# Performance work log

Measured on AMD Instinct MI355X. Metric: run time of the kernel, lower is better.

## Reference

```python
import jax, jax.numpy as jnp
import numpy as np

LMAX, MMAX = 6, 2
M_SIZE = (7, 6, 5)
SPHERE_C, HID = 128, 128
N_NODES, N_EDGES = 5000, 20000
N_COEFF_FULL = (LMAX + 1) ** 2                       # 49, l-primary node coeffs
N_COEFF_M = M_SIZE[0] + 2 * (M_SIZE[1] + M_SIZE[2])  # 29, m-primary edge coeffs
EXTRA_M0 = LMAX * HID                                # gate scalars from conv1


def _gate_idx():
    # maps each gated m-primary coefficient (all but l=0,m=0) to its degree index l-1
    idx = [l - 1 for l in range(1, LMAX + 1)]            # m=0 block (l=1..lmax)
    for m in range(1, MMAX + 1):
        for _ in range(2):                               # (-m, +m) components
            idx += [l - 1 for l in range(m, LMAX + 1)]
    return np.asarray(idx, dtype=np.int32)

GATE_IDX = jnp.asarray(_gate_idx())


def _layer_norm(h, s, b):
    mu = jnp.mean(h, axis=-1, keepdims=True)
    var = jnp.var(h, axis=-1, keepdims=True)
    return (h - mu) * jax.lax.rsqrt(var + 1e-5) * s + b


def _radial(e, w0, b0, s0, bb0, w1, b1, s1, bb1, w2, b2):
    h = jax.nn.silu(_layer_norm(e @ w0 + b0, s0, bb0))
    h = jax.nn.silu(_layer_norm(h @ w1 + b1, s1, bb1))
    return h @ w2 + b2


def _so2_conv(x, w_m0, b_m0, w_m1, w_m2, extra, x_rad=None):
    # x: [E, N_COEFF_M, C_in] in m-primary layout
    E = x.shape[0]
    w_m = (w_m1, w_m2)
    outs = []
    # m = 0: plain linear over flattened (l, channel)
    x0 = x[:, :M_SIZE[0]].reshape(E, -1)
    off_rad = 0
    if x_rad is not None:
        x0 = x0 * x_rad[:, :x0.shape[1]]
        off_rad = x0.shape[1]
    x0 = x0 @ w_m0 + b_m0
    x0_extra = None
    if extra:
        x0_extra, x0 = x0[:, :extra], x0[:, extra:]
    outs.append(x0.reshape(E, M_SIZE[0], -1))
    off = M_SIZE[0]
    # m > 0: complex-style SO(2) convolution per order m
    for m in range(1, MMAX + 1):
        sz = M_SIZE[m]
        xm = x[:, off:off + 2 * sz].reshape(E, 2, -1)    # [E, 2, sz*C_in]
        if x_rad is not None:
            d = xm.shape[2]
            xm = xm * x_rad[:, off_rad:off_rad + d][:, None, :]
            off_rad += d
        y = xm @ w_m[m - 1]                              # [E, 2, 2*sz*C_out]
        half = y.shape[2] // 2
        yr, yi = y[..., :half], y[..., half:]
        out_r = yr[:, 0] - yi[:, 1]
        out_i = yr[:, 1] + yi[:, 0]
        outs.append(jnp.stack((out_r, out_i), axis=1).reshape(E, 2 * sz, -1))
        off += 2 * sz
    out = jnp.concatenate(outs, axis=1)
    return (out, x0_extra) if extra else out


def _gate_act(gating, x):
    # gating: [E, LMAX*HID], x: [E, N_COEFF_M, HID]
    g = jax.nn.sigmoid(gating).reshape(-1, LMAX, HID)[:, GATE_IDX]  # [E, N_COEFF_M-1, HID]
    scalars = jax.nn.silu(x[:, :1])
    return jnp.concatenate((scalars, x[:, 1:] * g), axis=1)


def _edgewise(x, x_edge, edge_index, wig, wig_inv, env, params):
    (rw0, rb0, rs0, rbb0, rw1, rb1, rs1, rbb1, rw2, rb2,
     c1w0, c1b0, c1w1, c1w2, c2w0, c2b0, c2w1, c2w2) = params
    # gather source/target node features and concat channels -> [E, 49, 2C]
    msg = jnp.concatenate((x[edge_index[0]], x[edge_index[1]]), axis=2)
    # Wigner rotation + M mapping: l-primary (49) -> m-primary (29)
    msg = jnp.einsum('emj,ejc->emc', wig, msg)
    x_rad = _radial(x_edge, rw0, rb0, rs0, rbb0, rw1, rb1, rs1, rbb1, rw2, rb2)
    msg, gating = _so2_conv(msg, c1w0, c1b0, c1w1, c1w2, EXTRA_M0, x_rad)
    msg = _gate_act(gating, msg)
    msg = _so2_conv(msg, c2w0, c2b0, c2w1, c2w2, 0)
    msg = msg * env
    # inverse rotation: m-primary (29) -> l-primary (49)
    msg = jnp.einsum('ejm,emc->ejc', wig_inv, msg)
    return jax.ops.segment_sum(msg, edge_index[1], num_segments=x.shape[0])


def setup_inputs() -> dict:
    key = jax.random.key(0)
    ks = iter(jax.random.split(key, 40))
    def W(shape):
        return jax.random.normal(next(ks), shape, jnp.float32) / np.sqrt(shape[0])
    C_IN1 = 2 * SPHERE_C
    rad_out = C_IN1 * sum(M_SIZE)  # 4608
    inp = {}
    inp['x'] = jax.random.normal(next(ks), (N_NODES, N_COEFF_FULL, SPHERE_C), jnp.float32)
    inp['x_edge'] = jax.random.normal(next(ks), (N_EDGES, 128), jnp.float32)
    inp['edge_distance'] = jax.random.uniform(next(ks), (N_EDGES,), jnp.float32, 0.1, 6.0)
    inp['edge_index'] = jax.random.randint(next(ks), (2, N_EDGES), 0, N_NODES)
    inp['wigner_and_M_mapping'] = jax.random.normal(next(ks), (N_EDGES, N_COEFF_M, N_COEFF_FULL), jnp.float32) / np.sqrt(N_COEFF_FULL)
    inp['wigner_and_M_mapping_inv'] = jax.random.normal(next(ks), (N_EDGES, N_COEFF_FULL, N_COEFF_M), jnp.float32) / np.sqrt(N_COEFF_M)
    inp['edge_envelope'] = jax.random.uniform(next(ks), (N_EDGES, 1, 1), jnp.float32)
    inp['rad_w0'] = W((128, 256)); inp['rad_b0'] = jnp.zeros((256,), jnp.float32)
    inp['rad_ln0_s'] = jnp.ones((256,), jnp.float32); inp['rad_ln0_b'] = jnp.zeros((256,), jnp.float32)
    inp['rad_w1'] = W((256, 256)); inp['rad_b1'] = jnp.zeros((256,), jnp.float32)
    inp['rad_ln1_s'] = jnp.ones((256,), jnp.float32); inp['rad_ln1_b'] = jnp.zeros((256,), jnp.float32)
    inp['rad_w2'] = W((256, rad_out)); inp['rad_b2'] = jnp.zeros((rad_out,), jnp.float32)
    inp['c1_w_m0'] = W((M_SIZE[0] * C_IN1, M_SIZE[0] * HID + EXTRA_M0))
    inp['c1_b_m0'] = jnp.zeros((M_SIZE[0] * HID + EXTRA_M0,), jnp.float32)
    inp['c1_w_m1'] = W((M_SIZE[1] * C_IN1, 2 * M_SIZE[1] * HID))
    inp['c1_w_m2'] = W((M_SIZE[2] * C_IN1, 2 * M_SIZE[2] * HID))
    inp['c2_w_m0'] = W((M_SIZE[0] * HID, M_SIZE[0] * SPHERE_C))
    inp['c2_b_m0'] = jnp.zeros((M_SIZE[0] * SPHERE_C,), jnp.float32)
    inp['c2_w_m1'] = W((M_SIZE[1] * HID, 2 * M_SIZE[1] * SPHERE_C))
    inp['c2_w_m2'] = W((M_SIZE[2] * HID, 2 * M_SIZE[2] * SPHERE_C))
    return inp


def reference(x, x_edge, edge_distance, edge_index, wigner_and_M_mapping,
              wigner_and_M_mapping_inv, edge_envelope,
              rad_w0, rad_b0, rad_ln0_s, rad_ln0_b, rad_w1, rad_b1, rad_ln1_s, rad_ln1_b,
              rad_w2, rad_b2, c1_w_m0, c1_b_m0, c1_w_m1, c1_w_m2,
              c2_w_m0, c2_b_m0, c2_w_m1, c2_w_m2):
    # edge_distance is accepted (module signature) but unused in the original forward
    params = (rad_w0, rad_b0, rad_ln0_s, rad_ln0_b, rad_w1, rad_b1, rad_ln1_s, rad_ln1_b,
              rad_w2, rad_b2, c1_w_m0, c1_b_m0, c1_w_m1, c1_w_m2,
              c2_w_m0, c2_b_m0, c2_w_m1, c2_w_m2)
    return _edgewise(x, x_edge, edge_index, wigner_and_M_mapping,
                     wigner_and_M_mapping_inv, edge_envelope, params)
```

## Files before the change

kernel.cpp:

```cpp
#include <hip/hip_runtime.h>
#include <stdint.h>


#define E_NUM   20000
#define NN      5000

typedef uint16_t u16;
typedef __bf16  bf16x8 __attribute__((ext_vector_type(8)));
typedef float   f32x4  __attribute__((ext_vector_type(4)));
typedef uint16_t u16x8 __attribute__((ext_vector_type(8)));

__device__ __forceinline__ float bf2f(u16 h){
  uint32_t u = ((uint32_t)h) << 16;
  return __builtin_bit_cast(float, u);
}
__device__ __forceinline__ u16 f2bf(float f){
  uint32_t u = __builtin_bit_cast(uint32_t, f);
  u += 0x7fffu + ((u >> 16) & 1u);
  return (u16)(u >> 16);
}
__device__ __forceinline__ float sigm(float x){ return 1.f / (1.f + __expf(-x)); }

__device__ __forceinline__ void gload16(const void* g, void* l){
  __builtin_amdgcn_global_load_lds(
      (const __attribute__((address_space(1))) void*)g,
      (__attribute__((address_space(3))) void*)l, 16, 0, 0);
}

__device__ __forceinline__ int swz8(int orig, int nwg){
  int q = nwg >> 3, r = nwg & 7;
  int x = orig & 7, p = orig >> 3;
  int base = (x < r) ? x * (q + 1) : r * (q + 1) + (x - r) * q;
  return base + p;
}

__global__ void k_hist(const int* __restrict__ eidx, int* __restrict__ cnt){
  int e = blockIdx.x * 256 + threadIdx.x;
  if (e < E_NUM) atomicAdd(&cnt[eidx[E_NUM + e]], 1);
}
__global__ __launch_bounds__(256) void k_scan(const int* __restrict__ cnt,
                                              int* __restrict__ off){
  __shared__ int part[256];
  int t = threadIdx.x;
  int s = 0;
  #pragma unroll
  for (int i = 0; i < 20; ++i){
    int idx = t * 20 + i;
    if (idx < NN) s += cnt[idx];
  }
  part[t] = s;
  __syncthreads();
  if (t == 0){
    int run = 0;
    for (int i = 0; i < 256; ++i){ int v = part[i]; part[i] = run; run += v; }
  }
  __syncthreads();
  int run = part[t];
  #pragma unroll
  for (int i = 0; i < 20; ++i){
    int idx = t * 20 + i;
    if (idx < NN){ off[idx] = run; run += cnt[idx]; }
  }
}
__global__ void k_scatter(const int* __restrict__ eidx, int* __restrict__ off,
                          int* __restrict__ perm){
  int e = blockIdx.x * 256 + threadIdx.x;
  if (e < E_NUM){
    int pos = atomicAdd(&off[eidx[E_NUM + e]], 1);
    perm[pos] = e;
  }
}

__global__ void k_transpose_w(const float* __restrict__ in, u16* __restrict__ out,
                              int K, int N){
  __shared__ float t[32][33];
  int nb = blockIdx.x * 32, kb = blockIdx.y * 32;
  int tx = threadIdx.x & 31, ty = threadIdx.x >> 5;
  for (int i = ty; i < 32; i += 8)
    t[i][tx] = in[(size_t)(kb + i) * N + (nb + tx)];
  __syncthreads();
  for (int i = ty; i < 32; i += 8)
    out[(size_t)(nb + i) * K + (kb + tx)] = f2bf(t[tx][i]);
}

__global__ __launch_bounds__(256) void k_xpose(const float* __restrict__ x,
                                               u16* __restrict__ xT){
  __shared__ float t[6272];
  int n = blockIdx.x, tid = threadIdx.x;
  const float* xp = x + (size_t)n * 6272;
  for (int i = tid; i < 6272; i += 256) t[i] = xp[i];
  __syncthreads();
  int c = tid >> 1;
  int kh = (tid & 1) * 32;
  u16* o = xT + (size_t)n * 8192 + c * 64 + kh;
  #pragma unroll
  for (int q = 0; q < 4; ++q){
    u16x8 h;
    #pragma unroll
    for (int i = 0; i < 8; ++i){
      int k = kh + q * 8 + i;
      h[i] = (k < 49) ? f2bf(t[k * 128 + c]) : (u16)0;
    }
    *(u16x8*)(o + q * 8) = h;
  }
}

__global__ void k_gather_xe(const float* __restrict__ x_edge,
                            const int* __restrict__ perm,
                            u16* __restrict__ xe, int e0){
  int el = blockIdx.x, c = threadIdx.x;
  int pe = perm[e0 + el];
  xe[(size_t)el * 128 + c] = f2bf(x_edge[(size_t)pe * 128 + c]);
}

struct Seg {
  const u16* A; const u16* B; u16* C; const float* bias;
  int M, N, K, lda, blk0;
};
struct Seg5 { Seg s[5]; int nwg; };

__device__ __forceinline__ void gemm_tile(
    const u16* __restrict__ A, int lda, const u16* __restrict__ B,
    const float* __restrict__ bias, float* __restrict__ Cf,
    u16* __restrict__ Cb, int ldc, int M, int N, int K,
    int bm, int bn, u16* As , u16* Bs )
{
  const int tid  = threadIdx.x;
  const int lane = tid & 63;
  const int wave = tid >> 6;
  const int wm = wave >> 1, wn = wave & 1;
  const int fr = lane & 15, fq = lane >> 4;
  const int row0 = bm * 128;

  const int lr  = lane >> 2;
  const int lg  = lane & 3;
  const int rA0 = wave * 32 + lr;
  const int rA1 = rA0 + 16;
  const int g0  = lg ^ ((rA0 >> 1) & 3);
  const int g1  = lg ^ ((rA1 >> 1) & 3);
  int gra0 = row0 + rA0; if (gra0 > M - 1) gra0 = M - 1;
  int gra1 = row0 + rA1; if (gra1 > M - 1) gra1 = M - 1;
  const u16* aS0 = A + (size_t)gra0 * lda + g0 * 8;
  const u16* aS1 = A + (size_t)gra1 * lda + g1 * 8;
  const u16* bS0 = B + (size_t)(bn * 128 + rA0) * K + g0 * 8;
  const u16* bS1 = B + (size_t)(bn * 128 + rA1) * K + g1 * 8;
  const int dA0 = (wave * 32) * 32;
  const int dA1 = (wave * 32 + 16) * 32;

  int aoff[4], boff[4];
  #pragma unroll
  for (int mi = 0; mi < 4; ++mi){
    int r = wm * 64 + mi * 16 + fr;
    aoff[mi] = r * 32 + (fq ^ ((r >> 1) & 3)) * 8;
  }
  #pragma unroll
  for (int ni = 0; ni < 4; ++ni){
    int r = wn * 64 + ni * 16 + fr;
    boff[ni] = r * 32 + (fq ^ ((r >> 1) & 3)) * 8;
  }

  f32x4 acc[4][4];
  #pragma unroll
  for (int i = 0; i < 4; ++i)
    #pragma unroll
    for (int j = 0; j < 4; ++j) acc[i][j] = (f32x4){0.f, 0.f, 0.f, 0.f};

  auto stage = [&](int buf, int k0){
    gload16(aS0 + k0, &As[buf * 4096 + dA0]);
    gload16(aS1 + k0, &As[buf * 4096 + dA1]);
    gload16(bS0 + k0, &Bs[buf * 4096 + dA0]);
    gload16(bS1 + k0, &Bs[buf * 4096 + dA1]);
  };

  stage(0, 0);
  __syncthreads();
  int cur = 0;
  for (int k0 = 0; k0 < K; k0 += 32){
    if (k0 + 32 < K) stage(cur ^ 1, k0 + 32);
    bf16x8 af[4], bfv[4];
    #pragma unroll
    for (int mi = 0; mi < 4; ++mi)
      af[mi] = __builtin_bit_cast(bf16x8, *(const u16x8*)&As[cur * 4096 + aoff[mi]]);
    #pragma unroll
    for (int ni = 0; ni < 4; ++ni)
      bfv[ni] = __builtin_bit_cast(bf16x8, *(const u16x8*)&Bs[cur * 4096 + boff[ni]]);
    #pragma unroll
    for (int mi = 0; mi < 4; ++mi)
      #pragma unroll
      for (int ni = 0; ni < 4; ++ni)
        acc[mi][ni] = __builtin_amdgcn_mfma_f32_16x16x32_bf16(af[mi], bfv[ni], acc[mi][ni], 0, 0, 0);
    __syncthreads();
    cur ^= 1;
  }

  #pragma unroll
  for (int ni = 0; ni < 4; ++ni){
    int col = bn * 128 + wn * 64 + ni * 16 + fr;
    float bv = bias ? bias[col] : 0.f;
    #pragma unroll
    for (int mi = 0; mi < 4; ++mi){
      #pragma unroll
      for (int i = 0; i < 4; ++i){
        int row = row0 + wm * 64 + mi * 16 + fq * 4 + i;
        if (row < M){
          float v = acc[mi][ni][i] + bv;
          if (Cb) Cb[(size_t)row * ldc + col] = f2bf(v);
          else    Cf[(size_t)row * ldc + col] = v;
        }
      }
    }
  }
}

__global__ __launch_bounds__(256) void k_gemm_bt(
    const u16* __restrict__ A, int lda, const u16* __restrict__ B,
    const float* __restrict__ bias, float* __restrict__ Cf,
    u16* __restrict__ Cb, int ldc, int M, int N, int K)
{
  __shared__ u16 As[2 * 4096];
  __shared__ u16 Bs[2 * 4096];
  gemm_tile(A, lda, B, bias, Cf, Cb, ldc, M, N, K,
            blockIdx.y, blockIdx.x, As, Bs);
}

__global__ __launch_bounds__(256) void k_gemm_seg(Seg5 g)
{
  __shared__ u16 As[2 * 4096];
  __shared__ u16 Bs[2 * 4096];
  int wgid = swz8(blockIdx.x, g.nwg);
  Seg sg = g.s[4];
  if (wgid < g.s[4].blk0) sg = g.s[3];
  if (wgid < g.s[3].blk0) sg = g.s[2];
  if (wgid < g.s[2].blk0) sg = g.s[1];
  if (wgid < g.s[1].blk0) sg = g.s[0];
  int local = wgid - sg.blk0;
  int nbx = sg.N >> 7;
  int bn = local % nbx;
  int bm = local / nbx;
  gemm_tile(sg.A, sg.lda, sg.B, sg.bias, nullptr, sg.C, sg.N,
            sg.M, sg.N, sg.K, bm, bn, As, Bs);
}

__global__ __launch_bounds__(256) void k_ln_silu(
    const float* __restrict__ in, const float* __restrict__ sc,
    const float* __restrict__ bb, u16* __restrict__ out)
{
  int e = blockIdx.x, t = threadIdx.x;
  float v = in[(size_t)e * 256 + t];
  float s1 = v, s2 = v * v;
  #pragma unroll
  for (int off = 32; off > 0; off >>= 1){
    s1 += __shfl_down(s1, off);
    s2 += __shfl_down(s2, off);
  }
  __shared__ float r1[4], r2[4];
  if ((t & 63) == 0){ r1[t >> 6] = s1; r2[t >> 6] = s2; }
  __syncthreads();
  float S1 = r1[0] + r1[1] + r1[2] + r1[3];
  float S2 = r2[0] + r2[1] + r2[2] + r2[3];
  float mu  = S1 * (1.f / 256.f);
  float var = S2 * (1.f / 256.f) - mu * mu;
  float nv = (v - mu) * rsqrtf(var + 1e-5f) * sc[t] + bb[t];
  out[(size_t)e * 256 + t] = f2bf(nv * sigm(nv));
}

__global__ __launch_bounds__(256) void k_wig_fwd(
    const u16* __restrict__ xT, const int* __restrict__ eidx,
    const float* __restrict__ wig, const u16* __restrict__ xrad,
    u16* __restrict__ msgS, const int* __restrict__ perm, int e0)
{
  __shared__ u16 WL[32 * 64];
  int el = blockIdx.x, tid = threadIdx.x;
  int eg = perm[e0 + el];
  int lane = tid & 63, w = tid >> 6;

  const float* wp = wig + (size_t)eg * 1421;
  for (int idx = tid; idx < 2048; idx += 256){
    int m = idx >> 6, k = idx & 63;
    float v = (m < 29 && k < 49) ? wp[m * 49 + k] : 0.f;
    WL[m * 64 + ((((k >> 3) ^ (m & 7))) << 3) + (k & 7)] = f2bf(v);
  }

  const int fr = lane & 15, fq = lane >> 4;
  const int colbase = w * 64;
  int node = eidx[((w >> 1) ? E_NUM : 0) + eg];
  const u16* xb = xT + (size_t)node * 8192;
  bf16x8 bfv[4][2];
  #pragma unroll
  for (int ct = 0; ct < 4; ++ct)
    #pragma unroll
    for (int ks = 0; ks < 2; ++ks){
      int cc = ((w & 1) * 64) + ct * 16 + fr;
      bfv[ct][ks] = __builtin_bit_cast(bf16x8,
          *(const u16x8*)(xb + cc * 64 + (ks * 4 + fq) * 8));
    }
  __syncthreads();

  bf16x8 af[2][2];
  #pragma unroll
  for (int mt = 0; mt < 2; ++mt)
    #pragma unroll
    for (int ks = 0; ks < 2; ++ks){
      int m = mt * 16 + fr;
      int g = ks * 4 + fq;
      af[mt][ks] = __builtin_bit_cast(bf16x8,
          *(const u16x8*)&WL[m * 64 + ((g ^ (m & 7)) << 3)]);
    }
  f32x4 acc[2][4];
  #pragma unroll
  for (int mt = 0; mt < 2; ++mt)
    #pragma unroll
    for (int ct = 0; ct < 4; ++ct) acc[mt][ct] = (f32x4){0.f,0.f,0.f,0.f};
  #pragma unroll
  for (int mt = 0; mt < 2; ++mt)
    #pragma unroll
    for (int ct = 0; ct < 4; ++ct)
      #pragma unroll
      for (int ks = 0; ks < 2; ++ks)
        acc[mt][ct] = __builtin_amdgcn_mfma_f32_16x16x32_bf16(
            af[mt][ks], bfv[ct][ks], acc[mt][ct], 0, 0, 0);

  const u16* xr = xrad + (size_t)el * 4608;
  u16* o = msgS + (size_t)el * 7424;
  #pragma unroll
  for (int mt = 0; mt < 2; ++mt)
    #pragma unroll
    for (int ct = 0; ct < 4; ++ct){
      int col = colbase + ct * 16 + fr;
      #pragma unroll
      for (int r = 0; r < 4; ++r){
        int m = mt * 16 + fq * 4 + r;
        if (m < 29){
          int rr = (m < 13) ? m : (m < 24 ? m - 6 : m - 11);
          o[m * 256 + col] = f2bf(acc[mt][ct][r] * bf2f(xr[rr * 256 + col]));
        }
      }
    }
}

__global__ __launch_bounds__(256) void k_gate(
    const u16* __restrict__ c1m0, const u16* __restrict__ y10, const u16* __restrict__ y11,
    const u16* __restrict__ y20, const u16* __restrict__ y21, u16* __restrict__ msg2)
{
  int e = blockIdx.x, t = threadIdx.x;
  __shared__ float g[768];
  const u16* gp = c1m0 + (size_t)e * 1664;
  if (t < 96){
    u16x8 v = *(const u16x8*)(gp + t * 8);
    #pragma unroll
    for (int i = 0; i < 8; ++i) g[t * 8 + i] = sigm(bf2f(v[i]));
  }
  __syncthreads();
  const u16* x0 = gp + 768;
  const u16* a0 = y10 + (size_t)e * 1536;
  const u16* a1 = y11 + (size_t)e * 1536;
  const u16* b0 = y20 + (size_t)e * 1280;
  const u16* b1 = y21 + (size_t)e * 1280;
  u16* o = msg2 + (size_t)e * 3712;
  const int grp = (t & 15) * 8;
  for (int r = t >> 4; r < 29; r += 16){
    u16x8 outv;
    if (r == 0){
      u16x8 v = *(const u16x8*)(x0 + grp);
      #pragma unroll
      for (int i = 0; i < 8; ++i){ float f = bf2f(v[i]); outv[i] = f2bf(f * sigm(f)); }
    } else if (r < 7){
      u16x8 v = *(const u16x8*)(x0 + r * 128 + grp);
      #pragma unroll
      for (int i = 0; i < 8; ++i)
        outv[i] = f2bf(bf2f(v[i]) * g[(r - 1) * 128 + grp + i]);
    } else if (r < 19){
      int k = (r < 13) ? r - 7 : r - 13;
      u16x8 va = *(const u16x8*)(a0 + ((r < 13) ? k * 128 : 768 + k * 128) + grp);
      u16x8 vb = *(const u16x8*)(a1 + ((r < 13) ? 768 + k * 128 : k * 128) + grp);
      #pragma unroll
      for (int i = 0; i < 8; ++i){
        float fa = bf2f(va[i]), fb = bf2f(vb[i]);
        float val = (r < 13) ? (fa - fb) : (fb + fa);
        outv[i] = f2bf(val * g[k * 128 + grp + i]);
      }
    } else {
      int k = (r < 24) ? r - 19 : r - 24;
      u16x8 va = *(const u16x8*)(b0 + ((r < 24) ? k * 128 : 640 + k * 128) + grp);
      u16x8 vb = *(const u16x8*)(b1 + ((r < 24) ? 640 + k * 128 : k * 128) + grp);
      #pragma unroll
      for (int i = 0; i < 8; ++i){
        float fa = bf2f(va[i]), fb = bf2f(vb[i]);
        float val = (r < 24) ? (fa - fb) : (fb + fa);
        outv[i] = f2bf(val * g[(1 + k) * 128 + grp + i]);
      }
    }
    *(u16x8*)(o + r * 128 + grp) = outv;
  }
}

__global__ __launch_bounds__(128) void k_recomb2(
    const u16* __restrict__ m3x0, const u16* __restrict__ z10, const u16* __restrict__ z11,
    const u16* __restrict__ z20, const u16* __restrict__ z21, const float* __restrict__ env,
    u16* __restrict__ msg3T, const int* __restrict__ perm, int e0)
{
  __shared__ u16 s[6528];
  int e = blockIdx.x, c = threadIdx.x;
  {
    const u16* px0 = m3x0 + (size_t)e * 896;
    const u16* pa0 = z10 + (size_t)e * 1536;
    const u16* pa1 = z11 + (size_t)e * 1536;
    const u16* pb0 = z20 + (size_t)e * 1280;
    const u16* pb1 = z21 + (size_t)e * 1280;
    for (int v = c; v < 112; v += 128) *(u16x8*)(&s[v * 8])        = *(const u16x8*)(px0 + v * 8);
    for (int v = c; v < 192; v += 128) *(u16x8*)(&s[896 + v * 8])  = *(const u16x8*)(pa0 + v * 8);
    for (int v = c; v < 192; v += 128) *(u16x8*)(&s[2432 + v * 8]) = *(const u16x8*)(pa1 + v * 8);
    for (int v = c; v < 160; v += 128) *(u16x8*)(&s[3968 + v * 8]) = *(const u16x8*)(pb0 + v * 8);
    for (int v = c; v < 160; v += 128) *(u16x8*)(&s[5248 + v * 8]) = *(const u16x8*)(pb1 + v * 8);
  }
  __syncthreads();
  float ev = env[perm[e0 + e]];
  const u16* x0 = s;
  const u16* a0 = s + 896;
  const u16* a1 = s + 2432;
  const u16* b0 = s + 3968;
  const u16* b1 = s + 5248;
  u16 v[32];
  #pragma unroll
  for (int r = 0; r < 7; ++r) v[r] = f2bf(bf2f(x0[r * 128 + c]) * ev);
  #pragma unroll
  for (int k = 0; k < 6; ++k){
    float orr = bf2f(a0[k * 128 + c]) - bf2f(a1[768 + k * 128 + c]);
    float oii = bf2f(a1[k * 128 + c]) + bf2f(a0[768 + k * 128 + c]);
    v[7 + k]  = f2bf(orr * ev);
    v[13 + k] = f2bf(oii * ev);
  }
  #pragma unroll
  for (int k = 0; k < 5; ++k){
    float orr = bf2f(b0[k * 128 + c]) - bf2f(b1[640 + k * 128 + c]);
    float oii = bf2f(b1[k * 128 + c]) + bf2f(b0[640 + k * 128 + c]);
    v[19 + k] = f2bf(orr * ev);
    v[24 + k] = f2bf(oii * ev);
  }
  v[29] = 0; v[30] = 0; v[31] = 0;
  u16* o = msg3T + (size_t)e * 4096 + c * 32;
  #pragma unroll
  for (int q = 0; q < 4; ++q)
    *(u16x8*)(o + q * 8) = *(const u16x8*)(&v[q * 8]);
}

__global__ __launch_bounds__(256) void k_wig_inv(
    const u16* __restrict__ msg3T, const float* __restrict__ winv,
    const int* __restrict__ eidx, float* __restrict__ out,
    const int* __restrict__ perm, int e0, int cm)
{
  __shared__ u16 WV[64 * 32];
  int el = blockIdx.x, tid = threadIdx.x;
  int i = e0 + el;
  int d = eidx[E_NUM + perm[i]];
  if (el > 0 && eidx[E_NUM + perm[i - 1]] == d) return;
  bool tail = (el == 0) && (e0 > 0) && (eidx[E_NUM + perm[e0 - 1]] == d);
  int lane = tid & 63, w = tid >> 6;
  const int fr = lane & 15, fq = lane >> 4;
  const int jr = w * 16 + fr;

  f32x4 acc[8];
  #pragma unroll
  for (int ct = 0; ct < 8; ++ct) acc[ct] = (f32x4){0.f,0.f,0.f,0.f};

  int tend = e0 + cm;
  int t = i;
  for (; t < tend; ++t){
    int pe = perm[t];
    if (t > i && eidx[E_NUM + pe] != d) break;
    __syncthreads();
    const float* wp = winv + (size_t)pe * 1421;
    for (int idx = tid; idx < 2048; idx += 256){
      int j = idx >> 5, m = idx & 31;
      float v = (j < 49 && m < 29) ? wp[j * 29 + m] : 0.f;
      WV[j * 32 + (((m >> 3) ^ (j & 3)) << 3) + (m & 7)] = f2bf(v);
    }
    __syncthreads();
    bf16x8 a = __builtin_bit_cast(bf16x8,
        *(const u16x8*)&WV[jr * 32 + ((fq ^ (jr & 3)) << 3)]);
    const u16* bp = msg3T + (size_t)(t - e0) * 4096;
    #pragma unroll
    for (int ct = 0; ct < 8; ++ct){
      bf16x8 b = __builtin_bit_cast(bf16x8,
          *(const u16x8*)(bp + (ct * 16 + fr) * 32 + fq * 8));
      acc[ct] = __builtin_amdgcn_mfma_f32_16x16x32_bf16(a, b, acc[ct], 0, 0, 0);
    }
  }
  bool head = (t == tend) && (tend < E_NUM) && (eidx[E_NUM + perm[tend]] == d);
  bool atom = tail || head;

  float* op = out + (size_t)d * 6272;
  if (atom){
    #pragma unroll
    for (int ct = 0; ct < 8; ++ct){
      int c = ct * 16 + fr;
      #pragma unroll
      for (int r = 0; r < 4; ++r){
        int j = w * 16 + fq * 4 + r;
        if (j < 49) atomicAdd(op + j * 128 + c, acc[ct][r]);
      }
    }
  } else {
    #pragma unroll
    for (int ct = 0; ct < 8; ++ct){
      int c = ct * 16 + fr;
      #pragma unroll
      for (int r = 0; r < 4; ++r){
        int j = w * 16 + fq * 4 + r;
        if (j < 49) op[j * 128 + c] = acc[ct][r];
      }
    }
  }
}

extern "C" void kernel_launch(void* const* d_in, const int* in_sizes, int n_in,
                              void* d_out, int out_size, void* d_ws, size_t ws_size,
                              hipStream_t stream)
{
  (void)in_sizes; (void)n_in;
  const float* x       = (const float*)d_in[0];
  const float* x_edge  = (const float*)d_in[1];
  const int*   eidx    = (const int*)d_in[3];
  const float* wig     = (const float*)d_in[4];
  const float* wig_inv = (const float*)d_in[5];
  const float* env     = (const float*)d_in[6];
  const float* rad_w0  = (const float*)d_in[7];
  const float* rad_b0  = (const float*)d_in[8];
  const float* ln0_s   = (const float*)d_in[9];
  const float* ln0_b   = (const float*)d_in[10];
  const float* rad_w1  = (const float*)d_in[11];
  const float* rad_b1  = (const float*)d_in[12];
  const float* ln1_s   = (const float*)d_in[13];
  const float* ln1_b   = (const float*)d_in[14];
  const float* rad_w2  = (const float*)d_in[15];
  const float* rad_b2  = (const float*)d_in[16];
  const float* c1w0    = (const float*)d_in[17];
  const float* c1b0    = (const float*)d_in[18];
  const float* c1w1    = (const float*)d_in[19];
  const float* c1w2    = (const float*)d_in[20];
  const float* c2w0    = (const float*)d_in[21];
  const float* c2b0    = (const float*)d_in[22];
  const float* c2w1    = (const float*)d_in[23];
  const float* c2w2    = (const float*)d_in[24];
  float* out = (float*)d_out;

  char* base = (char*)d_ws;
  size_t off = 0;
  auto alloc = [&](size_t bytes) -> char* {
    off = (off + 255) & ~(size_t)255;
    char* r = base + off;
    off += bytes;
    return r;
  };

  u16* wtR0  = (u16*)alloc((size_t)256  * 128  * 2);
  u16* wtR1  = (u16*)alloc((size_t)256  * 256  * 2);
  u16* wtR2  = (u16*)alloc((size_t)4608 * 256  * 2);
  u16* wtC10 = (u16*)alloc((size_t)1664 * 1792 * 2);
  u16* wtC11 = (u16*)alloc((size_t)1536 * 1536 * 2);
  u16* wtC12 = (u16*)alloc((size_t)1280 * 1280 * 2);
  u16* wtC20 = (u16*)alloc((size_t)896  * 896  * 2);
  u16* wtC21 = (u16*)alloc((size_t)1536 * 768  * 2);
  u16* wtC22 = (u16*)alloc((size_t)1280 * 640  * 2);
  u16* xT    = (u16*)alloc((size_t)NN * 8192 * 2);
  int* cnt   = (int*)alloc(NN * 4);
  int* soff  = (int*)alloc(NN * 4);
  int* perm  = (int*)alloc(E_NUM * 4);

  size_t fixed_end = (off + 65536) & ~(size_t)65535;
  size_t avail = (ws_size > fixed_end + (1u << 20)) ? (ws_size - fixed_end - (1u << 20)) : 0;
  long CH0 = (long)(avail / 40960);
  if (CH0 > E_NUM) CH0 = E_NUM;
  if (CH0 < 64) CH0 = 64;
  int nch = (int)((E_NUM + CH0 - 1) / CH0);
  int CH = (E_NUM + nch - 1) / nch;
  if (CH > CH0) CH = (int)CH0;

  off = fixed_end;
  const size_t C = (size_t)CH;
  u16*   xe   = (u16*)alloc(C * 128 * 2);
  float* tmp  = (float*)alloc(C * 256 * 4);
  u16*   h0   = (u16*)alloc(C * 256 * 2);
  u16*   h1   = (u16*)alloc(C * 256 * 2);
  u16* region1 = (u16*)alloc(C * 4608 * 2);
  u16* region2 = (u16*)alloc(C * 7424 * 2);
  u16* region3 = (u16*)alloc(C * 7296 * 2);
  u16* xrad = region1;
  u16* msg2 = region1;
  u16* msgS = region2;
  u16* m3x0 = region2;
  u16* z10  = region2 + C * 896;
  u16* z11  = region2 + C * 2432;
  u16* z20  = region2 + C * 3968;
  u16* z21  = region2 + C * 5248;
  u16* c1m0b = region3;
  u16* y10   = region3 + C * 1664;
  u16* y11   = region3 + C * 3200;
  u16* y20   = region3 + C * 4736;
  u16* y21   = region3 + C * 6016;
  u16* msg3T = region3;

  hipMemsetAsync(d_out, 0, (size_t)out_size * sizeof(float), stream);
  hipMemsetAsync(cnt, 0, NN * 4, stream);

  k_hist<<<(E_NUM + 255) / 256, 256, 0, stream>>>(eidx, cnt);
  k_scan<<<1, 256, 0, stream>>>(cnt, soff);
  k_scatter<<<(E_NUM + 255) / 256, 256, 0, stream>>>(eidx, soff, perm);
  k_xpose<<<NN, 256, 0, stream>>>(x, xT);

  auto tw = [&](const float* in, u16* o, int K, int N){
    k_transpose_w<<<dim3(N / 32, K / 32), 256, 0, stream>>>(in, o, K, N);
  };
  tw(rad_w0, wtR0, 128, 256);
  tw(rad_w1, wtR1, 256, 256);
  tw(rad_w2, wtR2, 256, 4608);
  tw(c1w0, wtC10, 1792, 1664);
  tw(c1w1, wtC11, 1536, 1536);
  tw(c1w2, wtC12, 1280, 1280);
  tw(c2w0, wtC20, 896, 896);
  tw(c2w1, wtC21, 768, 1536);
  tw(c2w2, wtC22, 640, 1280);

  auto gemm = [&](const u16* A, int lda, const u16* B, const float* bias,
                  float* Cf, u16* Cb, int ldc, int M, int N, int K){
    k_gemm_bt<<<dim3(N / 128, (M + 127) / 128), 256, 0, stream>>>(
        A, lda, B, bias, Cf, Cb, ldc, M, N, K);
  };

  for (int e0 = 0; e0 < E_NUM; e0 += CH){
    int cm = E_NUM - e0 < CH ? E_NUM - e0 : CH;
    int mb = (cm + 127) / 128;

    k_gather_xe<<<cm, 128, 0, stream>>>(x_edge, perm, xe, e0);

    gemm(xe, 128, wtR0, rad_b0, tmp, nullptr, 256, cm, 256, 128);
    k_ln_silu<<<cm, 256, 0, stream>>>(tmp, ln0_s, ln0_b, h0);
    gemm(h0, 256, wtR1, rad_b1, tmp, nullptr, 256, cm, 256, 256);
    k_ln_silu<<<cm, 256, 0, stream>>>(tmp, ln1_s, ln1_b, h1);
    gemm(h1, 256, wtR2, rad_b2, nullptr, xrad, 4608, cm, 4608, 256);

    k_wig_fwd<<<cm, 256, 0, stream>>>(xT, eidx, wig, xrad, msgS, perm, e0);

    {
      Seg5 g;
      int b = 0;
      auto mk = [&](const u16* A, const u16* B, u16* Cb, const float* bias,
                    int N, int K) -> Seg {
        Seg s{A, B, Cb, bias, cm, N, K, 7424, b};
        b += (N >> 7) * mb;
        return s;
      };
      g.s[0] = mk(msgS,        wtC10, c1m0b, c1b0,   1664, 1792);
      g.s[1] = mk(msgS + 1792, wtC11, y10,   nullptr, 1536, 1536);
      g.s[2] = mk(msgS + 3328, wtC11, y11,   nullptr, 1536, 1536);
      g.s[3] = mk(msgS + 4864, wtC12, y20,   nullptr, 1280, 1280);
      g.s[4] = mk(msgS + 6144, wtC12, y21,   nullptr, 1280, 1280);
      g.nwg = b;
      k_gemm_seg<<<b, 256, 0, stream>>>(g);
    }

    k_gate<<<cm, 256, 0, stream>>>(c1m0b, y10, y11, y20, y21, msg2);

    {
      Seg5 g;
      int b = 0;
      auto mk = [&](const u16* A, const u16* B, u16* Cb, const float* bias,
                    int N, int K) -> Seg {
        Seg s{A, B, Cb, bias, cm, N, K, 3712, b};
        b += (N >> 7) * mb;
        return s;
      };
      g.s[0] = mk(msg2,        wtC20, m3x0, c2b0,   896,  896);
      g.s[1] = mk(msg2 + 896,  wtC21, z10,  nullptr, 1536, 768);
      g.s[2] = mk(msg2 + 1664, wtC21, z11,  nullptr, 1536, 768);
      g.s[3] = mk(msg2 + 2432, wtC22, z20,  nullptr, 1280, 640);
      g.s[4] = mk(msg2 + 3072, wtC22, z21,  nullptr, 1280, 640);
      g.nwg = b;
      k_gemm_seg<<<b, 256, 0, stream>>>(g);
    }

    k_recomb2<<<cm, 128, 0, stream>>>(m3x0, z10, z11, z20, z21, env, msg3T, perm, e0);

    k_wig_inv<<<cm, 256, 0, stream>>>(msg3T, wig_inv, eidx, out, perm, e0, cm);
  }
}
```

Baseline: 2.485 ms.

## Fuse radial GEMMs with LayerNorm+SiLU and restructure inverse Wigner scatter per node

Replaces the two radial-MLP GEMM plus separate LayerNorm/SiLU launches with a single 512-thread kernel that computes a full 256-wide row tile and applies bias, LayerNorm and SiLU in registers, removing the fp32 intermediate buffer round trip. The inverse Wigner kernel now launches one block per destination node, using the count and offset arrays to find each node's edge run instead of one block per edge with early exits. It also double-buffers the staged inverse-Wigner matrix so loading the next edge's weights overlaps the current MFMA work. The fused GEMM has fewer blocks (one per 128 rows), which may lower parallelism for the small radial GEMMs.

Result: faster. 2.356 ms (-5.2%).

```diff
diff --git a/kernel.cpp b/kernel.cpp
--- a/kernel.cpp
+++ b/kernel.cpp
@@ -241,27 +241,126 @@
             sg.M, sg.N, sg.K, bm, bn, As, Bs);
 }
 
-__global__ __launch_bounds__(256) void k_ln_silu(
-    const float* __restrict__ in, const float* __restrict__ sc,
-    const float* __restrict__ bb, u16* __restrict__ out)
-{
-  int e = blockIdx.x, t = threadIdx.x;
-  float v = in[(size_t)e * 256 + t];
-  float s1 = v, s2 = v * v;
-  #pragma unroll
-  for (int off = 32; off > 0; off >>= 1){
-    s1 += __shfl_down(s1, off);
-    s2 += __shfl_down(s2, off);
-  }
-  __shared__ float r1[4], r2[4];
-  if ((t & 63) == 0){ r1[t >> 6] = s1; r2[t >> 6] = s2; }
-  __syncthreads();
-  float S1 = r1[0] + r1[1] + r1[2] + r1[3];
-  float S2 = r2[0] + r2[1] + r2[2] + r2[3];
-  float mu  = S1 * (1.f / 256.f);
-  float var = S2 * (1.f / 256.f) - mu * mu;
-  float nv = (v - mu) * rsqrtf(var + 1e-5f) * sc[t] + bb[t];
-  out[(size_t)e * 256 + t] = f2bf(nv * sigm(nv));
+__global__ __launch_bounds__(512) void k_gemm_ln(
+    const u16* __restrict__ A, int lda, const u16* __restrict__ B ,
+    const float* __restrict__ bias, const float* __restrict__ lns,
+    const float* __restrict__ lnb, u16* __restrict__ out, int M, int K)
+{
+  __shared__ u16 As[2][4096];
+  __shared__ u16 Bs[2][8192];
+  __shared__ float rsum[128][4], rsq[128][4];
+  const int tid = threadIdx.x, lane = tid & 63, w = tid >> 6;
+  const int fr = lane & 15, fq = lane >> 4;
+  const int bm = blockIdx.x, row0 = bm * 128;
+
+  const int lr = lane >> 2, lg = lane & 3;
+  int rA = w * 16 + lr;
+  int gA = lg ^ ((rA >> 1) & 3);
+  int grA = row0 + rA; if (grA > M - 1) grA = M - 1;
+  const u16* aS = A + (size_t)grA * lda + gA * 8;
+  int rB0 = w * 32 + lr, rB1 = rB0 + 16;
+  int gB0 = lg ^ ((rB0 >> 1) & 3), gB1 = lg ^ ((rB1 >> 1) & 3);
+  const u16* bS0 = B + (size_t)rB0 * K + gB0 * 8;
+  const u16* bS1 = B + (size_t)rB1 * K + gB1 * 8;
+  const int dA  = (w * 16) * 32;
+  const int dB0 = (w * 32) * 32;
+  const int dB1 = (w * 32 + 16) * 32;
+
+  int aoff[4], boff[4];
+  #pragma unroll
+  for (int mi = 0; mi < 4; ++mi){
+    int r = (w & 1) * 64 + mi * 16 + fr;
+    aoff[mi] = r * 32 + (fq ^ ((r >> 1) & 3)) * 8;
+  }
+  #pragma unroll
+  for (int ni = 0; ni < 4; ++ni){
+    int ccol = (w >> 1) * 64 + ni * 16 + fr;
+    boff[ni] = ccol * 32 + (fq ^ ((ccol >> 1) & 3)) * 8;
+  }
+
+  f32x4 acc[4][4];
+  #pragma unroll
+  for (int i = 0; i < 4; ++i)
+    #pragma unroll
+    for (int j = 0; j < 4; ++j) acc[i][j] = (f32x4){0.f, 0.f, 0.f, 0.f};
+
+  auto stage = [&](int buf, int k0){
+    gload16(aS + k0, &As[buf][dA]);
+    gload16(bS0 + k0, &Bs[buf][dB0]);
+    gload16(bS1 + k0, &Bs[buf][dB1]);
+  };
+
+  stage(0, 0);
+  __syncthreads();
+  int cur = 0;
+  for (int k0 = 0; k0 < K; k0 += 32){
+    if (k0 + 32 < K) stage(cur ^ 1, k0 + 32);
+    bf16x8 af[4], bfv[4];
+    #pragma unroll
+    for (int mi = 0; mi < 4; ++mi)
+      af[mi] = __builtin_bit_cast(bf16x8, *(const u16x8*)&As[cur][aoff[mi]]);
+    #pragma unroll
+    for (int ni = 0; ni < 4; ++ni)
+      bfv[ni] = __builtin_bit_cast(bf16x8, *(const u16x8*)&Bs[cur][boff[ni]]);
+    #pragma unroll
+    for (int mi = 0; mi < 4; ++mi)
+      #pragma unroll
+      for (int ni = 0; ni < 4; ++ni)
+        acc[mi][ni] = __builtin_amdgcn_mfma_f32_16x16x32_bf16(af[mi], bfv[ni], acc[mi][ni], 0, 0, 0);
+    __syncthreads();
+    cur ^= 1;
+  }
+
+  const int cq = w >> 1;
+  float bv[4], sc[4], bb[4];
+  #pragma unroll
+  for (int ni = 0; ni < 4; ++ni){
+    int col = cq * 64 + ni * 16 + fr;
+    bv[ni] = bias[col]; sc[ni] = lns[col]; bb[ni] = lnb[col];
+  }
+  #pragma unroll
+  for (int mi = 0; mi < 4; ++mi){
+    #pragma unroll
+    for (int i = 0; i < 4; ++i){
+      float s1 = 0.f, s2 = 0.f;
+      #pragma unroll
+      for (int ni = 0; ni < 4; ++ni){
+        float v = acc[mi][ni][i] + bv[ni];
+        s1 += v; s2 += v * v;
+      }
+      #pragma unroll
+      for (int off = 1; off < 16; off <<= 1){
+        s1 += __shfl_xor(s1, off);
+        s2 += __shfl_xor(s2, off);
+      }
+      if (fr == 0){
+        int r = (w & 1) * 64 + mi * 16 + fq * 4 + i;
+        rsum[r][cq] = s1; rsq[r][cq] = s2;
+      }
+    }
+  }
+  __syncthreads();
+  #pragma unroll
+  for (int mi = 0; mi < 4; ++mi){
+    #pragma unroll
+    for (int i = 0; i < 4; ++i){
+      int r = (w & 1) * 64 + mi * 16 + fq * 4 + i;
+      float S1 = rsum[r][0] + rsum[r][1] + rsum[r][2] + rsum[r][3];
+      float S2 = rsq[r][0] + rsq[r][1] + rsq[r][2] + rsq[r][3];
+      float mu  = S1 * (1.f / 256.f);
+      float var = S2 * (1.f / 256.f) - mu * mu;
+      float rs  = rsqrtf(var + 1e-5f);
+      int row = row0 + r;
+      if (row < M){
+        #pragma unroll
+        for (int ni = 0; ni < 4; ++ni){
+          int col = cq * 64 + ni * 16 + fr;
+          float nv = (acc[mi][ni][i] + bv[ni] - mu) * rs * sc[ni] + bb[ni];
+          out[(size_t)row * 256 + col] = f2bf(nv * sigm(nv));
+        }
+      }
+    }
+  }
 }
 
 __global__ __launch_bounds__(256) void k_wig_fwd(
@@ -446,48 +545,54 @@
 
 __global__ __launch_bounds__(256) void k_wig_inv(
     const u16* __restrict__ msg3T, const float* __restrict__ winv,
-    const int* __restrict__ eidx, float* __restrict__ out,
-    const int* __restrict__ perm, int e0, int cm)
-{
-  __shared__ u16 WV[64 * 32];
-  int el = blockIdx.x, tid = threadIdx.x;
-  int i = e0 + el;
-  int d = eidx[E_NUM + perm[i]];
-  if (el > 0 && eidx[E_NUM + perm[i - 1]] == d) return;
-  bool tail = (el == 0) && (e0 > 0) && (eidx[E_NUM + perm[e0 - 1]] == d);
+    const int* __restrict__ cnt, const int* __restrict__ soff,
+    float* __restrict__ out, const int* __restrict__ perm, int e0, int cm)
+{
+  __shared__ u16 WV[2][2048];
+  int d = blockIdx.x, tid = threadIdx.x;
+  int cn = cnt[d];
+  if (cn == 0) return;
+  int runEnd = soff[d];
+  int runStart = runEnd - cn;
+  int start = runStart < e0 ? e0 : runStart;
+  int end   = runEnd > e0 + cm ? e0 + cm : runEnd;
+  if (start >= end) return;
+  bool atom = (start != runStart) || (end != runEnd);
+
   int lane = tid & 63, w = tid >> 6;
   const int fr = lane & 15, fq = lane >> 4;
   const int jr = w * 16 + fr;
 
-  f32x4 acc[8];
-  #pragma unroll
-  for (int ct = 0; ct < 8; ++ct) acc[ct] = (f32x4){0.f,0.f,0.f,0.f};
-
-  int tend = e0 + cm;
-  int t = i;
-  for (; t < tend; ++t){
-    int pe = perm[t];
-    if (t > i && eidx[E_NUM + pe] != d) break;
-    __syncthreads();
+  auto stageW = [&](int buf, int pe){
     const float* wp = winv + (size_t)pe * 1421;
     for (int idx = tid; idx < 2048; idx += 256){
       int j = idx >> 5, m = idx & 31;
       float v = (j < 49 && m < 29) ? wp[j * 29 + m] : 0.f;
-      WV[j * 32 + (((m >> 3) ^ (j & 3)) << 3) + (m & 7)] = f2bf(v);
+      WV[buf][j * 32 + (((m >> 3) ^ (j & 3)) << 3) + (m & 7)] = f2bf(v);
+    }
+  };
+
+  f32x4 acc[8];
+  #pragma unroll
+  for (int ct = 0; ct < 8; ++ct) acc[ct] = (f32x4){0.f,0.f,0.f,0.f};
+
+  stageW(0, perm[start]);
+  __syncthreads();
+  int b = 0;
+  for (int t = start; t < end; ++t){
+    if (t + 1 < end) stageW(b ^ 1, perm[t + 1]);
+    bf16x8 a = __builtin_bit_cast(bf16x8,
+        *(const u16x8*)&WV[b][jr * 32 + ((fq ^ (jr & 3)) << 3)]);
+    const u16* bp = msg3T + (size_t)(t - e0) * 4096;
+    #pragma unroll
+    for (int ct = 0; ct < 8; ++ct){
+      bf16x8 bo = __builtin_bit_cast(bf16x8,
+          *(const u16x8*)(bp + (ct * 16 + fr) * 32 + fq * 8));
+      acc[ct] = __builtin_amdgcn_mfma_f32_16x16x32_bf16(a, bo, acc[ct], 0, 0, 0);
     }
     __syncthreads();
-    bf16x8 a = __builtin_bit_cast(bf16x8,
-        *(const u16x8*)&WV[jr * 32 + ((fq ^ (jr & 3)) << 3)]);
-    const u16* bp = msg3T + (size_t)(t - e0) * 4096;
-    #pragma unroll
-    for (int ct = 0; ct < 8; ++ct){
-      bf16x8 b = __builtin_bit_cast(bf16x8,
-          *(const u16x8*)(bp + (ct * 16 + fr) * 32 + fq * 8));
-      acc[ct] = __builtin_amdgcn_mfma_f32_16x16x32_bf16(a, b, acc[ct], 0, 0, 0);
-    }
-  }
-  bool head = (t == tend) && (tend < E_NUM) && (eidx[E_NUM + perm[tend]] == d);
-  bool atom = tail || head;
+    b ^= 1;
+  }
 
   float* op = out + (size_t)d * 6272;
   if (atom){
@@ -579,7 +684,6 @@
   off = fixed_end;
   const size_t C = (size_t)CH;
   u16*   xe   = (u16*)alloc(C * 128 * 2);
-  float* tmp  = (float*)alloc(C * 256 * 4);
   u16*   h0   = (u16*)alloc(C * 256 * 2);
   u16*   h1   = (u16*)alloc(C * 256 * 2);
   u16* region1 = (u16*)alloc(C * 4608 * 2);
@@ -621,23 +725,16 @@
   tw(c2w1, wtC21, 768, 1536);
   tw(c2w2, wtC22, 640, 1280);
 
-  auto gemm = [&](const u16* A, int lda, const u16* B, const float* bias,
-                  float* Cf, u16* Cb, int ldc, int M, int N, int K){
-    k_gemm_bt<<<dim3(N / 128, (M + 127) / 128), 256, 0, stream>>>(
-        A, lda, B, bias, Cf, Cb, ldc, M, N, K);
-  };
-
   for (int e0 = 0; e0 < E_NUM; e0 += CH){
     int cm = E_NUM - e0 < CH ? E_NUM - e0 : CH;
     int mb = (cm + 127) / 128;
 
     k_gather_xe<<<cm, 128, 0, stream>>>(x_edge, perm, xe, e0);
 
-    gemm(xe, 128, wtR0, rad_b0, tmp, nullptr, 256, cm, 256, 128);
-    k_ln_silu<<<cm, 256, 0, stream>>>(tmp, ln0_s, ln0_b, h0);
-    gemm(h0, 256, wtR1, rad_b1, tmp, nullptr, 256, cm, 256, 256);
-    k_ln_silu<<<cm, 256, 0, stream>>>(tmp, ln1_s, ln1_b, h1);
-    gemm(h1, 256, wtR2, rad_b2, nullptr, xrad, 4608, cm, 4608, 256);
+    k_gemm_ln<<<mb, 512, 0, stream>>>(xe, 128, wtR0, rad_b0, ln0_s, ln0_b, h0, cm, 128);
+    k_gemm_ln<<<mb, 512, 0, stream>>>(h0, 256, wtR1, rad_b1, ln1_s, ln1_b, h1, cm, 256);
+    k_gemm_bt<<<dim3(4608 / 128, mb), 256, 0, stream>>>(
+        h1, 256, wtR2, rad_b2, nullptr, xrad, 4608, cm, 4608, 256);
 
     k_wig_fwd<<<cm, 256, 0, stream>>>(xT, eidx, wig, xrad, msgS, perm, e0);
 
@@ -681,6 +778,6 @@
 
     k_recomb2<<<cm, 128, 0, stream>>>(m3x0, z10, z11, z20, z21, env, msg3T, perm, e0);
 
-    k_wig_inv<<<cm, 256, 0, stream>>>(msg3T, wig_inv, eidx, out, perm, e0, cm);
-  }
-}
+    k_wig_inv<<<NN, 256, 0, stream>>>(msg3T, wig_inv, cnt, soff, out, perm, e0, cm);
+  }
+}
```
